# Performance work log

Hardware: AMD Instinct MI355X
Metric: run time of the kernel (lower is better)

Reference implementation:

```python
import jax, jax.numpy as jnp
import numpy as np

B, IMG, P, C_IN, D, NH, DEPTH, E, TOPK, NCLS = 8, 224, 16, 3, 768, 12, 12, 8, 2, 1000
DH = 4 * D
HD = D // NH
GRID = IMG // P
NPAT = GRID * GRID
MOE_POS = (1, 3, 5, 7, 9, 11)
N_DENSE = DEPTH - len(MOE_POS)
N_MOE = len(MOE_POS)


def setup_inputs() -> dict:
    key = jax.random.key(0)
    ks = iter(jax.random.split(key, 32))
    n = lambda shape: jax.random.normal(next(ks), shape, jnp.float32) * 0.02
    return dict(
        x=jax.random.normal(next(ks), (B, C_IN, IMG, IMG), jnp.float32),
        patch_w=n((D, C_IN * P * P)), patch_b=jnp.zeros((D,), jnp.float32),
        cls_token=n((1, 1, D)), pos_embed=n((1, NPAT + 1, D)),
        ln1_w=jnp.ones((DEPTH, D), jnp.float32), ln1_b=jnp.zeros((DEPTH, D), jnp.float32),
        qkv_w=n((DEPTH, 3 * D, D)), qkv_b=jnp.zeros((DEPTH, 3 * D), jnp.float32),
        proj_w=n((DEPTH, D, D)), proj_b=jnp.zeros((DEPTH, D), jnp.float32),
        ln2_w=jnp.ones((DEPTH, D), jnp.float32), ln2_b=jnp.zeros((DEPTH, D), jnp.float32),
        fc1_w=n((N_DENSE, DH, D)), fc1_b=jnp.zeros((N_DENSE, DH), jnp.float32),
        fc2_w=n((N_DENSE, D, DH)), fc2_b=jnp.zeros((N_DENSE, D), jnp.float32),
        gate_w=n((N_MOE, E, D)), gate_b=jnp.zeros((N_MOE, E), jnp.float32),
        exp_w1=n((N_MOE, E, DH, D)), exp_b1=jnp.zeros((N_MOE, E, DH), jnp.float32),
        exp_w2=n((N_MOE, E, D, DH)), exp_b2=jnp.zeros((N_MOE, E, D), jnp.float32),
        norm_w=jnp.ones((D,), jnp.float32), norm_b=jnp.zeros((D,), jnp.float32),
        head_w=n((NCLS, D)), head_b=jnp.zeros((NCLS,), jnp.float32),
    )


def _ln(x, w, b):
    m = x.mean(-1, keepdims=True)
    v = ((x - m) ** 2).mean(-1, keepdims=True)
    return (x - m) / jnp.sqrt(v + 1e-5) * w + b


def _attn(x, qw, qb, pw, pb):
    Bn, N, _ = x.shape
    qkv = (x @ qw.T + qb).reshape(Bn, N, 3, NH, HD).transpose(2, 0, 3, 1, 4)
    q, k, v = qkv[0], qkv[1], qkv[2]  # [B, NH, N, HD]
    a = jax.nn.softmax(jnp.einsum('bhnd,bhmd->bhnm', q, k) * HD ** -0.5, -1)
    o = jnp.einsum('bhnm,bhmd->bhnd', a, v).transpose(0, 2, 1, 3).reshape(Bn, N, D)
    return o @ pw.T + pb


def _moe(x, gw, gb, w1, b1, w2, b2):
    # FMoETransformerMLP with NaiveGate: top-2 routing, softmax over top-k logits.
    shp = x.shape
    xf = x.reshape(-1, D)  # [T, D]
    logits = xf @ gw.T + gb  # [T, E]
    vals, idx = jax.lax.top_k(logits, TOPK)
    sc = jax.nn.softmax(vals, -1)  # [T, TOPK]
    comb = (jax.nn.one_hot(idx, E, dtype=xf.dtype) * sc[..., None]).sum(1)  # [T, E]
    h = jax.nn.gelu(jnp.einsum('td,ehd->teh', xf, w1) + b1, approximate=False)
    y = jnp.einsum('teh,edh->ted', h, w2) + b2
    return (y * comb[..., None]).sum(1).reshape(shp)


def reference(x, patch_w, patch_b, cls_token, pos_embed, ln1_w, ln1_b, qkv_w, qkv_b, proj_w, proj_b, ln2_w, ln2_b, fc1_w, fc1_b, fc2_w, fc2_b, gate_w, gate_b, exp_w1, exp_b1, exp_w2, exp_b2, norm_w, norm_b, head_w, head_b):
    patches = x.reshape(B, C_IN, GRID, P, GRID, P).transpose(0, 2, 4, 1, 3, 5).reshape(B, NPAT, C_IN * P * P)
    z = jnp.concatenate([jnp.broadcast_to(cls_token, (B, 1, D)), patches @ patch_w.T + patch_b], 1) + pos_embed
    di = mi = 0
    for i in range(DEPTH):
        z = z + _attn(_ln(z, ln1_w[i], ln1_b[i]), qkv_w[i], qkv_b[i], proj_w[i], proj_b[i])
        h2 = _ln(z, ln2_w[i], ln2_b[i])
        if i in MOE_POS:
            z = z + _moe(h2, gate_w[mi], gate_b[mi], exp_w1[mi], exp_b1[mi], exp_w2[mi], exp_b2[mi])
            mi += 1
        else:
            z = z + (jax.nn.gelu(h2 @ fc1_w[di].T + fc1_b[di], approximate=False) @ fc2_w[di].T + fc2_b[di])
            di += 1
    z = _ln(z, norm_w, norm_b)
    return z[:, 0] @ head_w.T + head_b
```

## Files before the change

### kernel.cpp

```cpp
#include <hip/hip_runtime.h>
#include <hip/hip_bf16.h>
#include <math.h>

#define B_     8
#define IMG_   224
#define PATCH_ 16
#define CIN_   3
#define D_     768
#define NH_    12
#define DEPTH_ 12
#define NE_    8
#define NCLS_  1000
#define DH_    3072
#define HD_    64
#define GRD_   14
#define NPAT_  196
#define NTOK_  197
#define T_     (B_*NTOK_)
#define TP_    (B_*NPAT_)
#define NSLOT_ (T_*2)

typedef __bf16 bf16_t;
typedef __bf16 bf16x8 __attribute__((ext_vector_type(8)));
typedef __bf16 bf16x4 __attribute__((ext_vector_type(4)));
typedef float  f32x4  __attribute__((ext_vector_type(4)));

static __device__ __forceinline__ float gelu_f(float x){
    return 0.5f * x * (1.0f + erff(x * 0.70710678118654752440f));
}

__global__ __launch_bounds__(256) void k_cvt(const float* __restrict__ in,
                                             bf16_t* __restrict__ out, int n){
    int i = (blockIdx.x*256 + threadIdx.x)*8;
    if (i >= n) return;
    float4 a = *reinterpret_cast<const float4*>(in + i);
    float4 b = *reinterpret_cast<const float4*>(in + i + 4);
    bf16x8 h;
    h[0]=(bf16_t)a.x; h[1]=(bf16_t)a.y; h[2]=(bf16_t)a.z; h[3]=(bf16_t)a.w;
    h[4]=(bf16_t)b.x; h[5]=(bf16_t)b.y; h[6]=(bf16_t)b.z; h[7]=(bf16_t)b.w;
    *reinterpret_cast<bf16x8*>(out + i) = h;
}

__global__ void k_patch_gather(const float* __restrict__ x, bf16_t* __restrict__ pbuf){
    int idx = blockIdx.x*256 + threadIdx.x;
    if (idx >= TP_*D_) return;
    int k  = idx % D_;
    int tp = idx / D_;
    int p  = tp % NPAT_, b = tp / NPAT_;
    int c  = k >> 8;
    int ij = k & 255;
    int i  = ij >> 4, j = ij & 15;
    int gi = p / GRD_, gj = p % GRD_;
    pbuf[idx] = (bf16_t)x[(((size_t)b*CIN_ + c)*IMG_ + gi*PATCH_ + i)*IMG_ + gj*PATCH_ + j];
}

template<int ACT, int GATHER, int MOE, int OUTBF, int KSPLIT, int PARTIAL>
__global__ __launch_bounds__(256) void k_mgemm(
    const bf16_t* __restrict__ A, const int* __restrict__ gidx,
    const bf16_t* __restrict__ W, const float* __restrict__ bias,
    void* __restrict__ Cout, int M, int N, int K,
    const int* __restrict__ moff, const int* __restrict__ mcnt)
{
    __shared__ __align__(16) bf16_t As[3][64*64];
    __shared__ __align__(16) bf16_t Bs[3][128*64];
    const int tid = threadIdx.x, lane = tid & 63, w = tid >> 6;
    int row_begin, Mhi, ksid;
    if (MOE) {
        const int e = blockIdx.z;
        const int o = moff[e], c = mcnt[e];
        const int rb = (KSPLIT == 2) ? (int)(blockIdx.y >> 1) : (int)blockIdx.y;
        ksid = (KSPLIT == 2) ? (int)(blockIdx.y & 1) : 0;
        row_begin = o + rb*64;
        Mhi = o + c;
        if (row_begin >= Mhi) return;
        W += (size_t)e*N*K;
        if (!PARTIAL) bias += (size_t)e*N;
    } else {
        row_begin = blockIdx.y*64;
        ksid = (KSPLIT == 2) ? (int)blockIdx.z : 0;
        Mhi = M;
    }
    const int bn = blockIdx.x*128;
    const int KL = K / KSPLIT;

    const bf16_t* aG[2];
    const bf16_t* wG[4];
    int aOff[2], wOff[4];
    #pragma unroll
    for (int i = 0; i < 2; ++i) {
        const int s = w*2 + i;
        const int row_l = s*8 + (lane >> 3);
        const int cc = (lane & 7) ^ (row_l & 7);
        const int gg = min(row_begin + row_l, Mhi - 1);
        const int tok = GATHER ? (gidx[gg] >> 1) : gg;
        aG[i] = A + (size_t)tok*K + ksid*KL + cc*8;
        aOff[i] = s*512;
    }
    #pragma unroll
    for (int j = 0; j < 4; ++j) {
        const int s = w*4 + j;
        const int row_l = s*8 + (lane >> 3);
        const int cc = (lane & 7) ^ (row_l & 7);
        wG[j] = W + (size_t)(bn + row_l)*K + ksid*KL + cc*8;
        wOff[j] = s*512;
    }
    const int wm = (w >> 1)*32, wn = (w & 1)*64;
    const int fr = lane & 15, kg = lane >> 4;
    int offA[2][2], offB[2][4];
    #pragma unroll
    for (int ks = 0; ks < 2; ++ks) {
        #pragma unroll
        for (int t = 0; t < 2; ++t) {
            const int ra = wm + t*16 + fr;
            offA[ks][t] = ra*128 + (((ks*4 + kg) ^ (ra & 7)) << 4);
        }
        #pragma unroll
        for (int t = 0; t < 4; ++t) {
            const int rb2 = wn + t*16 + fr;
            offB[ks][t] = rb2*128 + (((ks*4 + kg) ^ (rb2 & 7)) << 4);
        }
    }

    auto issue = [&](int sb) {
        #pragma unroll
        for (int i = 0; i < 2; ++i) {
            __builtin_amdgcn_global_load_lds(
                (const __attribute__((address_space(1))) void*)(aG[i]),
                (__attribute__((address_space(3))) void*)(&As[sb][aOff[i]]), 16, 0, 0);
            aG[i] += 64;
        }
        #pragma unroll
        for (int j = 0; j < 4; ++j) {
            __builtin_amdgcn_global_load_lds(
                (const __attribute__((address_space(1))) void*)(wG[j]),
                (__attribute__((address_space(3))) void*)(&Bs[sb][wOff[j]]), 16, 0, 0);
            wG[j] += 64;
        }
    };

    f32x4 acc[2][4] = {};
    const int nt = KL >> 6;
    issue(0);
    if (nt > 1) issue(1);
    int cur = 0, nxt2 = 2;
    for (int t = 0; t < nt; ++t) {
        if (t + 1 < nt) { asm volatile("s_waitcnt vmcnt(6)" ::: "memory"); }
        else            { asm volatile("s_waitcnt vmcnt(0)" ::: "memory"); }
        __builtin_amdgcn_sched_barrier(0);
        __builtin_amdgcn_s_barrier();
        __builtin_amdgcn_sched_barrier(0);
        if (t + 2 < nt) issue(nxt2);
        const char* baseA = (const char*)&As[cur][0];
        const char* baseB = (const char*)&Bs[cur][0];
        #pragma unroll
        for (int ks = 0; ks < 2; ++ks) {
            bf16x8 af[2], bf[4];
            #pragma unroll
            for (int t2 = 0; t2 < 2; ++t2)
                af[t2] = *reinterpret_cast<const bf16x8*>(baseA + offA[ks][t2]);
            #pragma unroll
            for (int t2 = 0; t2 < 4; ++t2)
                bf[t2] = *reinterpret_cast<const bf16x8*>(baseB + offB[ks][t2]);
            #pragma unroll
            for (int mt = 0; mt < 2; ++mt)
                #pragma unroll
                for (int nt2 = 0; nt2 < 4; ++nt2)
                    acc[mt][nt2] = __builtin_amdgcn_mfma_f32_16x16x32_bf16(
                        af[mt], bf[nt2], acc[mt][nt2], 0, 0, 0);
        }
        cur  = (cur  == 2) ? 0 : cur  + 1;
        nxt2 = (nxt2 == 2) ? 0 : nxt2 + 1;
    }
    float*  Cf = (float*)Cout + ((PARTIAL && KSPLIT == 2) ? (size_t)ksid*M*N : (size_t)0);
    bf16_t* Cb = (bf16_t*)Cout;
    const int cr = kg*4;
    #pragma unroll
    for (int nt2 = 0; nt2 < 4; ++nt2) {
        const int n = bn + wn + nt2*16 + fr;
        const float bv = PARTIAL ? 0.0f : bias[n];
        #pragma unroll
        for (int mt = 0; mt < 2; ++mt) {
            #pragma unroll
            for (int r2 = 0; r2 < 4; ++r2) {
                const int m = row_begin + wm + mt*16 + cr + r2;
                if (m < Mhi) {
                    float v = acc[mt][nt2][r2] + bv;
                    if (ACT) v = gelu_f(v);
                    if (OUTBF) Cb[(size_t)m*N + n] = (bf16_t)v;
                    else       Cf[(size_t)m*N + n] = v;
                }
            }
        }
    }
}

struct LNOut { float y0, y1, y2; };
static __device__ __forceinline__ LNOut ln_block(float v0, float v1, float v2,
        const float* __restrict__ w, const float* __restrict__ b,
        float* red, int tid)
{
    const int wid = tid >> 6, lane = tid & 63;
    float s = v0 + v1 + v2;
    for (int m=32;m>0;m>>=1) s += __shfl_xor(s, m);
    if (lane == 0) red[wid] = s;
    __syncthreads();
    if (tid == 0) red[4] = (red[0]+red[1]+red[2]+red[3]) * (1.0f/768.0f);
    __syncthreads();
    const float mean = red[4];
    float d0 = v0-mean, d1 = v1-mean, d2 = v2-mean;
    float q = d0*d0 + d1*d1 + d2*d2;
    for (int m=32;m>0;m>>=1) q += __shfl_xor(q, m);
    if (lane == 0) red[wid] = q;
    __syncthreads();
    if (tid == 0) {
        float var = (red[0]+red[1]+red[2]+red[3]) * (1.0f/768.0f);
        red[5] = 1.0f / sqrtf(var + 1e-5f);
    }
    __syncthreads();
    const float rstd = red[5];
    LNOut o;
    o.y0 = d0*rstd*w[tid    ] + b[tid    ];
    o.y1 = d1*rstd*w[tid+256] + b[tid+256];
    o.y2 = d2*rstd*w[tid+512] + b[tid+512];
    return o;
}

template<typename TOUT>
__global__ __launch_bounds__(256) void k_ln(const float* __restrict__ X,
        const float* __restrict__ w, const float* __restrict__ b,
        TOUT* __restrict__ Y, int in_mul)
{
    __shared__ float red[8];
    const int r = blockIdx.x, tid = threadIdx.x;
    const float* xr = X + (size_t)r*in_mul*D_;
    LNOut o = ln_block(xr[tid], xr[tid+256], xr[tid+512], w, b, red, tid);
    TOUT* yr = Y + (size_t)r*D_;
    yr[tid] = (TOUT)o.y0; yr[tid+256] = (TOUT)o.y1; yr[tid+512] = (TOUT)o.y2;
}

__global__ __launch_bounds__(256) void k_asmln(const float* __restrict__ pe,
        const float* __restrict__ cls, const float* __restrict__ pos,
        float* __restrict__ z, const float* __restrict__ w,
        const float* __restrict__ b, bf16_t* __restrict__ Y)
{
    __shared__ float red[8];
    const int t = blockIdx.x, tid = threadIdx.x;
    const int bb = t / NTOK_, r = t % NTOK_;
    float v[3];
    #pragma unroll
    for (int j = 0; j < 3; ++j) {
        const int n = tid + j*256;
        if (r == 0) v[j] = cls[n] + pos[n];
        else        v[j] = pe[((size_t)bb*NPAT_ + (r-1))*D_ + n] + pos[(size_t)r*D_ + n];
        z[(size_t)t*D_ + n] = v[j];
    }
    LNOut o = ln_block(v[0], v[1], v[2], w, b, red, tid);
    bf16_t* yr = Y + (size_t)t*D_;
    yr[tid] = (bf16_t)o.y0; yr[tid+256] = (bf16_t)o.y1; yr[tid+512] = (bf16_t)o.y2;
}

template<int GATE, int NP>
__global__ __launch_bounds__(256) void k_addln(
    float* __restrict__ z, const float* __restrict__ P,
    const float* __restrict__ bias,
    const float* __restrict__ w, const float* __restrict__ b,
    bf16_t* __restrict__ Y,
    const float* __restrict__ gw, const float* __restrict__ gb,
    int* __restrict__ t_e, float* __restrict__ t_sc)
{
    __shared__ float red[8];
    __shared__ float red2[4][8];
    const int t = blockIdx.x, tid = threadIdx.x;
    const int wid = tid >> 6, lane = tid & 63;
    const float* P1 = P + (size_t)T_*D_;
    float v[3];
    #pragma unroll
    for (int j = 0; j < 3; ++j) {
        const int n = tid + j*256;
        float nv = z[(size_t)t*D_+n] + P[(size_t)t*D_+n] + bias[n];
        if (NP == 2) nv += P1[(size_t)t*D_+n];
        z[(size_t)t*D_+n] = nv;
        v[j] = nv;
    }
    LNOut o = ln_block(v[0], v[1], v[2], w, b, red, tid);
    bf16_t* yr = Y + (size_t)t*D_;
    yr[tid] = (bf16_t)o.y0; yr[tid+256] = (bf16_t)o.y1; yr[tid+512] = (bf16_t)o.y2;
    if (GATE) {
        float p[NE_];
        #pragma unroll
        for (int e = 0; e < NE_; ++e)
            p[e] = o.y0*gw[e*D_+tid] + o.y1*gw[e*D_+tid+256] + o.y2*gw[e*D_+tid+512];
        #pragma unroll
        for (int e = 0; e < NE_; ++e)
            for (int m=32;m>0;m>>=1) p[e] += __shfl_xor(p[e], m);
        if (lane == 0)
            #pragma unroll
            for (int e = 0; e < NE_; ++e) red2[wid][e] = p[e];
        __syncthreads();
        if (tid == 0) {
            float l[NE_];
            #pragma unroll
            for (int e = 0; e < NE_; ++e)
                l[e] = red2[0][e]+red2[1][e]+red2[2][e]+red2[3][e] + gb[e];
            int i0 = 0;
            for (int e = 1; e < NE_; ++e) if (l[e] > l[i0]) i0 = e;
            int i1 = -1;
            for (int e = 0; e < NE_; ++e) if (e != i0 && (i1 < 0 || l[e] > l[i1])) i1 = e;
            float e1 = __expf(l[i1] - l[i0]);
            float s = 1.0f + e1;
            t_e[t*2]   = i0;   t_e[t*2+1]  = i1;
            t_sc[t*2]  = 1.0f/s; t_sc[t*2+1] = e1/s;
        }
    }
}

__global__ __launch_bounds__(1024) void k_scansc(const int* __restrict__ t_e,
        int* __restrict__ gidx, int* __restrict__ rg,
        int* __restrict__ offs, int* __restrict__ counts)
{
    __shared__ int h[NE_], o[NE_], c2[NE_];
    const int tid = threadIdx.x;
    if (tid < NE_) h[tid] = 0;
    __syncthreads();
    for (int id = tid; id < NSLOT_; id += 1024) atomicAdd(&h[t_e[id]], 1);
    __syncthreads();
    if (tid == 0) {
        int s = 0;
        for (int e = 0; e < NE_; ++e) { o[e] = s; s += h[e]; c2[e] = 0; }
    }
    __syncthreads();
    if (tid < NE_) { offs[tid] = o[tid]; counts[tid] = h[tid]; }
    for (int id = tid; id < NSLOT_; id += 1024) {
        int e = t_e[id];
        int pos = atomicAdd(&c2[e], 1);
        int g = o[e] + pos;
        gidx[g] = id;
        rg[id] = g;
    }
}

template<int LN>
__global__ __launch_bounds__(256) void k_comb(
    const float* __restrict__ mp, const float* __restrict__ b2,
    const int* __restrict__ t_e, const int* __restrict__ rg,
    const float* __restrict__ t_sc, float* __restrict__ z,
    const float* __restrict__ w, const float* __restrict__ b,
    bf16_t* __restrict__ Y)
{
    __shared__ float red[8];
    const int t = blockIdx.x, tid = threadIdx.x;
    const int g0 = rg[2*t], g1 = rg[2*t+1];
    const int e0 = t_e[2*t], e1 = t_e[2*t+1];
    const float s0 = t_sc[2*t], s1 = t_sc[2*t+1];
    const float* mp1 = mp + (size_t)NSLOT_*D_;
    float v[3];
    #pragma unroll
    for (int j = 0; j < 3; ++j) {
        const int n = tid + j*256;
        float y0 = mp[(size_t)g0*D_+n] + mp1[(size_t)g0*D_+n] + b2[(size_t)e0*D_+n];
        float y1 = mp[(size_t)g1*D_+n] + mp1[(size_t)g1*D_+n] + b2[(size_t)e1*D_+n];
        float nv = z[(size_t)t*D_+n] + s0*y0 + s1*y1;
        z[(size_t)t*D_+n] = nv;
        v[j] = nv;
    }
    if (LN) {
        LNOut o = ln_block(v[0], v[1], v[2], w, b, red, tid);
        bf16_t* yr = Y + (size_t)t*D_;
        yr[tid] = (bf16_t)o.y0; yr[tid+256] = (bf16_t)o.y1; yr[tid+512] = (bf16_t)o.y2;
    }
}

__global__ __launch_bounds__(256) void k_attn(const bf16_t* __restrict__ qkv,
                                              bf16_t* __restrict__ out)
{
    __shared__ bf16_t Kl[NTOK_*68];
    __shared__ float  qs[8][64];
    __shared__ bf16_t ps[8][200];
    const int qb = blockIdx.x*8;
    const int h = blockIdx.y, b = blockIdx.z;
    const int tid = threadIdx.x, lane = tid & 63, wid = tid >> 6;
    for (int id = tid; id < NTOK_*8; id += 256) {
        const int m = id >> 3, c = id & 7;
        bf16x8 v = *reinterpret_cast<const bf16x8*>(
            qkv + (size_t)(b*NTOK_+m)*2304 + 768 + h*HD_ + c*8);
        bf16x4 lo = {v[0],v[1],v[2],v[3]}, hi = {v[4],v[5],v[6],v[7]};
        *reinterpret_cast<bf16x4*>(&Kl[m*68 + c*8    ]) = lo;
        *reinterpret_cast<bf16x4*>(&Kl[m*68 + c*8 + 4]) = hi;
    }
    for (int id = tid; id < 512; id += 256) {
        const int qq = id >> 6, d = id & 63;
        const int n = qb + qq;
        qs[qq][d] = (n < NTOK_) ? (float)qkv[(size_t)(b*NTOK_+n)*2304 + h*HD_ + d] : 0.0f;
    }
    __syncthreads();
    const int na = qb + wid, nb = qb + wid + 4;
    const bool va = na < NTOK_, vb = nb < NTOK_;
    if (!va) return;
    float sa[4] = {0,0,0,0}, sb[4] = {0,0,0,0};
    for (int d = 0; d < HD_; d += 4) {
        const f32x4 qa = *reinterpret_cast<const f32x4*>(&qs[wid][d]);
        const f32x4 qv = *reinterpret_cast<const f32x4*>(&qs[wid+4][d]);
        #pragma unroll
        for (int j = 0; j < 4; ++j) {
            const int m = lane + 64*j;
            const int mc = m < NTOK_ ? m : NTOK_-1;
            bf16x4 kv = *reinterpret_cast<const bf16x4*>(&Kl[mc*68 + d]);
            float k0=(float)kv[0], k1=(float)kv[1], k2=(float)kv[2], k3=(float)kv[3];
            sa[j] += qa[0]*k0 + qa[1]*k1 + qa[2]*k2 + qa[3]*k3;
            sb[j] += qv[0]*k0 + qv[1]*k1 + qv[2]*k2 + qv[3]*k3;
        }
    }
    #pragma unroll
    for (int j = 0; j < 4; ++j) {
        const bool ok = (lane + 64*j) < NTOK_;
        sa[j] = ok ? sa[j]*0.125f : -3.0e38f;
        sb[j] = ok ? sb[j]*0.125f : -3.0e38f;
    }
    float mxa = fmaxf(fmaxf(sa[0],sa[1]), fmaxf(sa[2],sa[3]));
    float mxb = fmaxf(fmaxf(sb[0],sb[1]), fmaxf(sb[2],sb[3]));
    for (int m=32;m>0;m>>=1) { mxa = fmaxf(mxa, __shfl_xor(mxa,m)); mxb = fmaxf(mxb, __shfl_xor(mxb,m)); }
    float pa[4], pb[4], suma = 0.0f, sumb = 0.0f;
    #pragma unroll
    for (int j = 0; j < 4; ++j) {
        pa[j] = __expf(sa[j]-mxa); suma += pa[j];
        pb[j] = __expf(sb[j]-mxb); sumb += pb[j];
    }
    for (int m=32;m>0;m>>=1) { suma += __shfl_xor(suma,m); sumb += __shfl_xor(sumb,m); }
    #pragma unroll
    for (int j = 0; j < 4; ++j) {
        const int m = lane + 64*j;
        if (m < NTOK_) {
            ps[wid][m] = (bf16_t)pa[j];
            if (vb) ps[wid+4][m] = (bf16_t)pb[j];
        }
    }
    const float inva = 1.0f/suma, invb = 1.0f/sumb;
    const bf16_t* vbase = qkv + (size_t)b*NTOK_*2304 + 1536 + h*HD_ + lane;
    float aa = 0.0f, ab = 0.0f;
    if (vb) {
        for (int m = 0; m < NTOK_; ++m) {
            const float vv = (float)vbase[(size_t)m*2304];
            aa += (float)ps[wid][m]*vv;
            ab += (float)ps[wid+4][m]*vv;
        }
    } else {
        for (int m = 0; m < NTOK_; ++m)
            aa += (float)ps[wid][m]*(float)vbase[(size_t)m*2304];
    }
    out[(size_t)(b*NTOK_+na)*D_ + h*HD_ + lane] = (bf16_t)(aa*inva);
    if (vb) out[(size_t)(b*NTOK_+nb)*D_ + h*HD_ + lane] = (bf16_t)(ab*invb);
}

__global__ __launch_bounds__(256) void k_head(const float* __restrict__ zn,
        const float* __restrict__ hw, const float* __restrict__ hb,
        float* __restrict__ out)
{
    const int o = blockIdx.x*4 + (threadIdx.x >> 6);
    const int b = blockIdx.y;
    const int lane = threadIdx.x & 63;
    if (o >= NCLS_) return;
    float acc = 0.0f;
    #pragma unroll 4
    for (int k = lane; k < D_; k += 64)
        acc = fmaf(zn[b*D_+k], hw[(size_t)o*D_+k], acc);
    for (int m=32;m>0;m>>=1) acc += __shfl_xor(acc, m);
    if (lane == 0) out[b*NCLS_+o] = acc + hb[o];
}

extern "C" void kernel_launch(void* const* d_in, const int* in_sizes, int n_in,
                              void* d_out, int out_size, void* d_ws, size_t ws_size,
                              hipStream_t stream)
{
    const float* x        = (const float*)d_in[0];
    const float* patch_w  = (const float*)d_in[1];
    const float* patch_b  = (const float*)d_in[2];
    const float* cls_tok  = (const float*)d_in[3];
    const float* pos_emb  = (const float*)d_in[4];
    const float* ln1_w    = (const float*)d_in[5];
    const float* ln1_b    = (const float*)d_in[6];
    const float* qkv_w    = (const float*)d_in[7];
    const float* qkv_b    = (const float*)d_in[8];
    const float* proj_w   = (const float*)d_in[9];
    const float* proj_b   = (const float*)d_in[10];
    const float* ln2_w    = (const float*)d_in[11];
    const float* ln2_b    = (const float*)d_in[12];
    const float* fc1_w    = (const float*)d_in[13];
    const float* fc1_b    = (const float*)d_in[14];
    const float* fc2_w    = (const float*)d_in[15];
    const float* fc2_b    = (const float*)d_in[16];
    const float* gate_w   = (const float*)d_in[17];
    const float* gate_b   = (const float*)d_in[18];
    const float* exp_w1   = (const float*)d_in[19];
    const float* exp_b1   = (const float*)d_in[20];
    const float* exp_w2   = (const float*)d_in[21];
    const float* exp_b2   = (const float*)d_in[22];
    const float* norm_w   = (const float*)d_in[23];
    const float* norm_b   = (const float*)d_in[24];
    const float* head_w   = (const float*)d_in[25];
    const float* head_b   = (const float*)d_in[26];

    char* wsb = (char*)d_ws;
    size_t off_ = 0;
    auto alloc = [&](size_t nelem, size_t esz) -> void* {
        void* p = wsb + off_;
        off_ += ((nelem*esz + 255) / 256) * 256;
        return p;
    };
    float*  z      = (float*) alloc((size_t)T_*D_, 4);
    bf16_t* lnbuf  = (bf16_t*)alloc((size_t)T_*D_, 2);
    bf16_t* qkvbuf = (bf16_t*)alloc((size_t)T_*3*D_, 2);
    bf16_t* abuf   = (bf16_t*)alloc((size_t)T_*D_, 2);
    bf16_t* hid    = (bf16_t*)alloc((size_t)NSLOT_*DH_, 2);
    float*  pp     = (float*) alloc((size_t)2*T_*D_, 4);
    float*  mp     = (float*) alloc((size_t)2*NSLOT_*D_, 4);
    float*  t_sc   = (float*) alloc(NSLOT_, 4);
    float*  zn     = (float*) alloc((size_t)B_*D_, 4);
    int*    t_e    = (int*)   alloc(NSLOT_, 4);
    int*    rg     = (int*)   alloc(NSLOT_, 4);
    int*    gidx   = (int*)   alloc(NSLOT_, 4);
    int*    offs   = (int*)   alloc(8, 4);
    int*    counts = (int*)   alloc(8, 4);
    const size_t n_patch = (size_t)D_*D_;
    const size_t n_qkv   = (size_t)DEPTH_*3*D_*D_;
    const size_t n_proj  = (size_t)DEPTH_*D_*D_;
    const size_t n_fc1   = (size_t)6*DH_*D_;
    const size_t n_fc2   = (size_t)6*D_*DH_;
    const size_t n_e1    = (size_t)6*NE_*DH_*D_;
    const size_t n_e2    = (size_t)6*NE_*D_*DH_;
    bf16_t* wb_patch = (bf16_t*)alloc(n_patch, 2);
    bf16_t* wb_qkv   = (bf16_t*)alloc(n_qkv, 2);
    bf16_t* wb_proj  = (bf16_t*)alloc(n_proj, 2);
    bf16_t* wb_fc1   = (bf16_t*)alloc(n_fc1, 2);
    bf16_t* wb_fc2   = (bf16_t*)alloc(n_fc2, 2);
    bf16_t* wb_e1    = (bf16_t*)alloc(n_e1, 2);
    bf16_t* wb_e2    = (bf16_t*)alloc(n_e2, 2);
    bf16_t* pbuf   = hid;
    float*  pout   = mp;

    auto cvt = [&](const float* src, bf16_t* dst, size_t n){
        k_cvt<<<dim3((unsigned)((n/8 + 255)/256)), 256, 0, stream>>>(src, dst, (int)n);
    };
    cvt(patch_w, wb_patch, n_patch);
    cvt(qkv_w,   wb_qkv,   n_qkv);
    cvt(proj_w,  wb_proj,  n_proj);
    cvt(fc1_w,   wb_fc1,   n_fc1);
    cvt(fc2_w,   wb_fc2,   n_fc2);
    cvt(exp_w1,  wb_e1,    n_e1);
    cvt(exp_w2,  wb_e2,    n_e2);

    k_patch_gather<<<dim3((TP_*D_+255)/256), 256, 0, stream>>>(x, pbuf);
    k_mgemm<0,0,0,0,1,0><<<dim3(D_/128, (TP_+63)/64), 256, 0, stream>>>(
        pbuf, nullptr, wb_patch, patch_b, pout, TP_, D_, D_, nullptr, nullptr);
    k_asmln<<<T_, 256, 0, stream>>>(pout, cls_tok, pos_emb, z, ln1_w, ln1_b, lnbuf);

    const int GY = (T_+63)/64;
    int di = 0, mi = 0;
    for (int i = 0; i < DEPTH_; ++i){
        k_mgemm<0,0,0,1,1,0><<<dim3(3*D_/128, GY), 256, 0, stream>>>(
            lnbuf, nullptr, wb_qkv + (size_t)i*3*D_*D_, qkv_b + (size_t)i*3*D_,
            qkvbuf, T_, 3*D_, D_, nullptr, nullptr);
        k_attn<<<dim3((NTOK_+7)/8, NH_, B_), 256, 0, stream>>>(qkvbuf, abuf);
        k_mgemm<0,0,0,0,1,1><<<dim3(D_/128, GY), 256, 0, stream>>>(
            abuf, nullptr, wb_proj + (size_t)i*D_*D_, nullptr,
            pp, T_, D_, D_, nullptr, nullptr);
        if (i & 1){
            k_addln<1,1><<<T_, 256, 0, stream>>>(z, pp, proj_b + i*D_,
                ln2_w + i*D_, ln2_b + i*D_, lnbuf,
                gate_w + (size_t)mi*NE_*D_, gate_b + (size_t)mi*NE_, t_e, t_sc);
            k_scansc<<<1, 1024, 0, stream>>>(t_e, gidx, rg, offs, counts);
            k_mgemm<1,1,1,1,1,0><<<dim3(DH_/128, 50, NE_), 256, 0, stream>>>(
                lnbuf, gidx, wb_e1 + (size_t)mi*NE_*DH_*D_, exp_b1 + (size_t)mi*NE_*DH_,
                hid, NSLOT_, DH_, D_, offs, counts);
            k_mgemm<0,0,1,0,2,1><<<dim3(D_/128, 100, NE_), 256, 0, stream>>>(
                hid, nullptr, wb_e2 + (size_t)mi*NE_*D_*DH_, nullptr,
                mp, NSLOT_, D_, DH_, offs, counts);
            if (i + 1 < DEPTH_) {
                k_comb<1><<<T_, 256, 0, stream>>>(mp, exp_b2 + (size_t)mi*NE_*D_,
                    t_e, rg, t_sc, z, ln1_w + (i+1)*D_, ln1_b + (i+1)*D_, lnbuf);
            } else {
                k_comb<0><<<T_, 256, 0, stream>>>(mp, exp_b2 + (size_t)mi*NE_*D_,
                    t_e, rg, t_sc, z, nullptr, nullptr, nullptr);
            }
            mi++;
        } else {
            k_addln<0,1><<<T_, 256, 0, stream>>>(z, pp, proj_b + i*D_,
                ln2_w + i*D_, ln2_b + i*D_, lnbuf,
                nullptr, nullptr, nullptr, nullptr);
            k_mgemm<1,0,0,1,1,0><<<dim3(DH_/128, GY), 256, 0, stream>>>(
                lnbuf, nullptr, wb_fc1 + (size_t)di*DH_*D_, fc1_b + (size_t)di*DH_,
                hid, T_, DH_, D_, nullptr, nullptr);
            k_mgemm<0,0,0,0,2,1><<<dim3(D_/128, GY, 2), 256, 0, stream>>>(
                hid, nullptr, wb_fc2 + (size_t)di*D_*DH_, nullptr,
                pp, T_, D_, DH_, nullptr, nullptr);
            k_addln<0,2><<<T_, 256, 0, stream>>>(z, pp, fc2_b + di*D_,
                ln1_w + (i+1)*D_, ln1_b + (i+1)*D_, lnbuf,
                nullptr, nullptr, nullptr, nullptr);
            di++;
        }
    }
    k_ln<float><<<B_, 256, 0, stream>>>(z, norm_w, norm_b, zn, NTOK_);
    k_head<<<dim3((NCLS_+3)/4, B_), 256, 0, stream>>>(zn, head_w, head_b, (float*)d_out);
}
```

Baseline: 2.897 ms.

## Template GEMM on M-tile and wave count, drop triple-buffered pipeline

```diff
diff --git a/kernel.cpp b/kernel.cpp
--- a/kernel.cpp
+++ b/kernel.cpp
@@ -54,15 +54,15 @@
     pbuf[idx] = (bf16_t)x[(((size_t)b*CIN_ + c)*IMG_ + gi*PATCH_ + i)*IMG_ + gj*PATCH_ + j];
 }
 
-template<int ACT, int GATHER, int MOE, int OUTBF, int KSPLIT, int PARTIAL>
-__global__ __launch_bounds__(256) void k_mgemm(
+template<int ACT, int GATHER, int MOE, int OUTBF, int KSPLIT, int PARTIAL, int BMT, int NW>
+__global__ __launch_bounds__(NW*64) void k_mgemm(
     const bf16_t* __restrict__ A, const int* __restrict__ gidx,
     const bf16_t* __restrict__ W, const float* __restrict__ bias,
     void* __restrict__ Cout, int M, int N, int K,
     const int* __restrict__ moff, const int* __restrict__ mcnt)
 {
-    __shared__ __align__(16) bf16_t As[3][64*64];
-    __shared__ __align__(16) bf16_t Bs[3][128*64];
+    __shared__ __align__(16) bf16_t As[BMT*64];
+    __shared__ __align__(16) bf16_t Bs[128*64];
     const int tid = threadIdx.x, lane = tid & 63, w = tid >> 6;
     int row_begin, Mhi, ksid;
     if (MOE) {
@@ -70,13 +70,13 @@
         const int o = moff[e], c = mcnt[e];
         const int rb = (KSPLIT == 2) ? (int)(blockIdx.y >> 1) : (int)blockIdx.y;
         ksid = (KSPLIT == 2) ? (int)(blockIdx.y & 1) : 0;
-        row_begin = o + rb*64;
+        row_begin = o + rb*BMT;
         Mhi = o + c;
         if (row_begin >= Mhi) return;
         W += (size_t)e*N*K;
         if (!PARTIAL) bias += (size_t)e*N;
     } else {
-        row_begin = blockIdx.y*64;
+        row_begin = blockIdx.y*BMT;
         ksid = (KSPLIT == 2) ? (int)blockIdx.z : 0;
         Mhi = M;
     }
@@ -84,8 +84,7 @@
     const int KL = K / KSPLIT;
 
     const bf16_t* aG[2];
-    const bf16_t* wG[4];
-    int aOff[2], wOff[4];
+    int aOff[2];
     #pragma unroll
     for (int i = 0; i < 2; ++i) {
         const int s = w*2 + i;
@@ -96,9 +95,12 @@
         aG[i] = A + (size_t)tok*K + ksid*KL + cc*8;
         aOff[i] = s*512;
     }
-    #pragma unroll
-    for (int j = 0; j < 4; ++j) {
-        const int s = w*4 + j;
+    constexpr int NB = 16/NW;
+    const bf16_t* wG[NB];
+    int wOff[NB];
+    #pragma unroll
+    for (int j = 0; j < NB; ++j) {
+        const int s = w*NB + j;
         const int row_l = s*8 + (lane >> 3);
         const int cc = (lane & 7) ^ (row_l & 7);
         wG[j] = W + (size_t)(bn + row_l)*K + ksid*KL + cc*8;
@@ -121,37 +123,27 @@
         }
     }
 
-    auto issue = [&](int sb) {
+    f32x4 acc[2][4] = {};
+    const int nt = KL >> 6;
+    for (int t = 0; t < nt; ++t) {
+        if (t) __syncthreads();
         #pragma unroll
         for (int i = 0; i < 2; ++i) {
             __builtin_amdgcn_global_load_lds(
                 (const __attribute__((address_space(1))) void*)(aG[i]),
-                (__attribute__((address_space(3))) void*)(&As[sb][aOff[i]]), 16, 0, 0);
+                (__attribute__((address_space(3))) void*)(&As[aOff[i]]), 16, 0, 0);
             aG[i] += 64;
         }
         #pragma unroll
-        for (int j = 0; j < 4; ++j) {
+        for (int j = 0; j < NB; ++j) {
             __builtin_amdgcn_global_load_lds(
                 (const __attribute__((address_space(1))) void*)(wG[j]),
-                (__attribute__((address_space(3))) void*)(&Bs[sb][wOff[j]]), 16, 0, 0);
+                (__attribute__((address_space(3))) void*)(&Bs[wOff[j]]), 16, 0, 0);
             wG[j] += 64;
         }
-    };
-
-    f32x4 acc[2][4] = {};
-    const int nt = KL >> 6;
-    issue(0);
-    if (nt > 1) issue(1);
-    int cur = 0, nxt2 = 2;
-    for (int t = 0; t < nt; ++t) {
-        if (t + 1 < nt) { asm volatile("s_waitcnt vmcnt(6)" ::: "memory"); }
-        else            { asm volatile("s_waitcnt vmcnt(0)" ::: "memory"); }
-        __builtin_amdgcn_sched_barrier(0);
-        __builtin_amdgcn_s_barrier();
-        __builtin_amdgcn_sched_barrier(0);
-        if (t + 2 < nt) issue(nxt2);
-        const char* baseA = (const char*)&As[cur][0];
-        const char* baseB = (const char*)&Bs[cur][0];
+        __syncthreads();
+        const char* baseA = (const char*)&As[0];
+        const char* baseB = (const char*)&Bs[0];
         #pragma unroll
         for (int ks = 0; ks < 2; ++ks) {
             bf16x8 af[2], bf[4];
@@ -168,8 +160,6 @@
                     acc[mt][nt2] = __builtin_amdgcn_mfma_f32_16x16x32_bf16(
                         af[mt], bf[nt2], acc[mt][nt2], 0, 0, 0);
         }
-        cur  = (cur  == 2) ? 0 : cur  + 1;
-        nxt2 = (nxt2 == 2) ? 0 : nxt2 + 1;
     }
     float*  Cf = (float*)Cout + ((PARTIAL && KSPLIT == 2) ? (size_t)ksid*M*N : (size_t)0);
     bf16_t* Cb = (bf16_t*)Cout;
@@ -549,18 +539,19 @@
     cvt(exp_w2,  wb_e2,    n_e2);
 
     k_patch_gather<<<dim3((TP_*D_+255)/256), 256, 0, stream>>>(x, pbuf);
-    k_mgemm<0,0,0,0,1,0><<<dim3(D_/128, (TP_+63)/64), 256, 0, stream>>>(
+    k_mgemm<0,0,0,0,1,0,64,4><<<dim3(D_/128, (TP_+63)/64), 256, 0, stream>>>(
         pbuf, nullptr, wb_patch, patch_b, pout, TP_, D_, D_, nullptr, nullptr);
     k_asmln<<<T_, 256, 0, stream>>>(pout, cls_tok, pos_emb, z, ln1_w, ln1_b, lnbuf);
 
-    const int GY = (T_+63)/64;
+    const int GY64  = (T_+63)/64;
+    const int GY128 = (T_+127)/128;
     int di = 0, mi = 0;
     for (int i = 0; i < DEPTH_; ++i){
-        k_mgemm<0,0,0,1,1,0><<<dim3(3*D_/128, GY), 256, 0, stream>>>(
+        k_mgemm<0,0,0,1,1,0,64,4><<<dim3(3*D_/128, GY64), 256, 0, stream>>>(
             lnbuf, nullptr, wb_qkv + (size_t)i*3*D_*D_, qkv_b + (size_t)i*3*D_,
             qkvbuf, T_, 3*D_, D_, nullptr, nullptr);
         k_attn<<<dim3((NTOK_+7)/8, NH_, B_), 256, 0, stream>>>(qkvbuf, abuf);
-        k_mgemm<0,0,0,0,1,1><<<dim3(D_/128, GY), 256, 0, stream>>>(
+        k_mgemm<0,0,0,0,1,1,64,4><<<dim3(D_/128, GY64), 256, 0, stream>>>(
             abuf, nullptr, wb_proj + (size_t)i*D_*D_, nullptr,
             pp, T_, D_, D_, nullptr, nullptr);
         if (i & 1){
@@ -568,10 +559,10 @@
                 ln2_w + i*D_, ln2_b + i*D_, lnbuf,
                 gate_w + (size_t)mi*NE_*D_, gate_b + (size_t)mi*NE_, t_e, t_sc);
             k_scansc<<<1, 1024, 0, stream>>>(t_e, gidx, rg, offs, counts);
-            k_mgemm<1,1,1,1,1,0><<<dim3(DH_/128, 50, NE_), 256, 0, stream>>>(
+            k_mgemm<1,1,1,1,1,0,128,8><<<dim3(DH_/128, 25, NE_), 512, 0, stream>>>(
                 lnbuf, gidx, wb_e1 + (size_t)mi*NE_*DH_*D_, exp_b1 + (size_t)mi*NE_*DH_,
                 hid, NSLOT_, DH_, D_, offs, counts);
-            k_mgemm<0,0,1,0,2,1><<<dim3(D_/128, 100, NE_), 256, 0, stream>>>(
+            k_mgemm<0,0,1,0,2,1,128,8><<<dim3(D_/128, 50, NE_), 512, 0, stream>>>(
                 hid, nullptr, wb_e2 + (size_t)mi*NE_*D_*DH_, nullptr,
                 mp, NSLOT_, D_, DH_, offs, counts);
             if (i + 1 < DEPTH_) {
@@ -586,10 +577,10 @@
             k_addln<0,1><<<T_, 256, 0, stream>>>(z, pp, proj_b + i*D_,
                 ln2_w + i*D_, ln2_b + i*D_, lnbuf,
                 nullptr, nullptr, nullptr, nullptr);
-            k_mgemm<1,0,0,1,1,0><<<dim3(DH_/128, GY), 256, 0, stream>>>(
+            k_mgemm<1,0,0,1,1,0,128,8><<<dim3(DH_/128, GY128), 512, 0, stream>>>(
                 lnbuf, nullptr, wb_fc1 + (size_t)di*DH_*D_, fc1_b + (size_t)di*DH_,
                 hid, T_, DH_, D_, nullptr, nullptr);
-            k_mgemm<0,0,0,0,2,1><<<dim3(D_/128, GY, 2), 256, 0, stream>>>(
+            k_mgemm<0,0,0,0,2,1,64,4><<<dim3(D_/128, GY64, 2), 256, 0, stream>>>(
                 hid, nullptr, wb_fc2 + (size_t)di*D_*DH_, nullptr,
                 pp, T_, D_, DH_, nullptr, nullptr);
             k_addln<0,2><<<T_, 256, 0, stream>>>(z, pp, fc2_b + di*D_,
```

Result: faster. 2.659 ms (-8.2%).
